# Kernel tuning notes

Measured on AMD Instinct MI355X. Metric: run time of the kernel, lower is better.

The kernel has to match this reference:

```python
import jax, jax.numpy as jnp
import numpy as np

N_NODES = 10000

def setup_inputs() -> dict:
    key = jax.random.key(0)
    k1, k2, k3, k4, k5 = jax.random.split(key, 5)
    n_edges = 640000
    d_in = 128
    d_out = 128
    x = jax.random.normal(k1, (N_NODES, d_in), dtype=jnp.float32)
    src = jax.random.randint(k2, (n_edges,), 0, N_NODES, dtype=jnp.int32)
    dst = jax.random.randint(k3, (n_edges,), 0, N_NODES, dtype=jnp.int32)
    W = jax.random.normal(k4, (d_in, d_out), dtype=jnp.float32) * (1.0 / np.sqrt(d_in))
    b = jax.random.normal(k5, (d_out,), dtype=jnp.float32) * 0.01
    return {"x": x, "src": src, "dst": dst, "W": W, "b": b}

def reference(x, src, dst, W, b):
    # copy_src + sum reduce: for each edge, send x[src]; each node sums incoming msgs
    msgs = x[src]  # [E, d_in] gather
    h = jax.ops.segment_sum(msgs, dst, num_segments=N_NODES)  # [N, d_in] scatter-add
    # dropout p=0.0 -> identity; linear + relu
    out = jax.nn.relu(h @ W + b)  # [N, d_out]
    return out
```

## Files before the change

### kernel.cpp

```cpp
#include <hip/hip_runtime.h>

#define N_NODES 10000
#define D 128
#define N_EDGES 640000
#define SHARDS 8
#define CSTRIDE 10016
#define BCAP 32
#define GEMM_BLOCKS 313
#define FILL_BLOCKS 2500

__device__ __forceinline__ unsigned short f2bf(float f) {
  unsigned int u = __float_as_uint(f);
  unsigned int r = (u + 0x7fffu + ((u >> 16) & 1u)) >> 16;
  return (unsigned short)r;
}
__device__ __forceinline__ float bf2f(unsigned short s) {
  return __uint_as_float((unsigned int)s << 16);
}

__global__ __launch_bounds__(256) void gcn_gemm_histfill_kernel(
    const float* __restrict__ x, const float* __restrict__ W,
    unsigned short* __restrict__ xw,
    const int* __restrict__ src, const int* __restrict__ dst,
    int* __restrict__ counts, unsigned short* __restrict__ srcs_pad) {
  __shared__ unsigned short Wl[D * D];

  if (blockIdx.x >= GEMM_BLOCKS) {
    int e = (blockIdx.x - GEMM_BLOCKS) * 256 + threadIdx.x;
    if (e < N_EDGES) {
      int d = dst[e];
      int s = src[e];
      int sh = blockIdx.x & (SHARDS - 1);
      int r = atomicAdd(&counts[sh * CSTRIDE + d], 1);
      if (r < BCAP)
        srcs_pad[((size_t)d * SHARDS + sh) * BCAP + r] = (unsigned short)s;
    }
    return;
  }

  for (int i = threadIdx.x; i < D * D; i += 256) Wl[i] = f2bf(W[i]);
  __syncthreads();

  const int c0 = (threadIdx.x & 31) * 4;
  const int r0 = blockIdx.x * 32 + (threadIdx.x >> 5) * 4;
  if (r0 >= N_NODES) return;

  float4 acc0 = {0, 0, 0, 0}, acc1 = acc0, acc2 = acc0, acc3 = acc0;
  const float* x0 = x + (size_t)r0 * D;

#define GEMM_STEP(J, HC)                                              \
  {                                                                   \
    ushort4 wu = *(const ushort4*)&Wl[(k4 + J) * D + c0];             \
    float wx = bf2f(wu.x), wy = bf2f(wu.y);                           \
    float wz = bf2f(wu.z), ww = bf2f(wu.w);                           \
    acc0.x = fmaf(hv0.HC, wx, acc0.x);                                \
    acc0.y = fmaf(hv0.HC, wy, acc0.y);                                \
    acc0.z = fmaf(hv0.HC, wz, acc0.z);                                \
    acc0.w = fmaf(hv0.HC, ww, acc0.w);                                \
    acc1.x = fmaf(hv1.HC, wx, acc1.x);                                \
    acc1.y = fmaf(hv1.HC, wy, acc1.y);                                \
    acc1.z = fmaf(hv1.HC, wz, acc1.z);                                \
    acc1.w = fmaf(hv1.HC, ww, acc1.w);                                \
    acc2.x = fmaf(hv2.HC, wx, acc2.x);                                \
    acc2.y = fmaf(hv2.HC, wy, acc2.y);                                \
    acc2.z = fmaf(hv2.HC, wz, acc2.z);                                \
    acc2.w = fmaf(hv2.HC, ww, acc2.w);                                \
    acc3.x = fmaf(hv3.HC, wx, acc3.x);                                \
    acc3.y = fmaf(hv3.HC, wy, acc3.y);                                \
    acc3.z = fmaf(hv3.HC, wz, acc3.z);                                \
    acc3.w = fmaf(hv3.HC, ww, acc3.w);                                \
  }

  for (int k4 = 0; k4 < D; k4 += 4) {
    float4 hv0 = *(const float4*)(x0 + 0 * D + k4);
    float4 hv1 = *(const float4*)(x0 + 1 * D + k4);
    float4 hv2 = *(const float4*)(x0 + 2 * D + k4);
    float4 hv3 = *(const float4*)(x0 + 3 * D + k4);
    GEMM_STEP(0, x)
    GEMM_STEP(1, y)
    GEMM_STEP(2, z)
    GEMM_STEP(3, w)
  }
#undef GEMM_STEP

  ushort4 sv;
#define STORE_ROW(R, ACC)                                              \
  sv.x = f2bf(ACC.x); sv.y = f2bf(ACC.y);                              \
  sv.z = f2bf(ACC.z); sv.w = f2bf(ACC.w);                              \
  *(ushort4*)(xw + (size_t)(r0 + R) * D + c0) = sv;
  STORE_ROW(0, acc0)
  STORE_ROW(1, acc1)
  STORE_ROW(2, acc2)
  STORE_ROW(3, acc3)
#undef STORE_ROW
}

__global__ __launch_bounds__(256) void gcn_gather_kernel(
    const unsigned short* __restrict__ xw, const int* __restrict__ counts,
    const unsigned short* __restrict__ srcs_pad,
    const float* __restrict__ b, float* __restrict__ out) {
  const int node = blockIdx.x * 4 + (threadIdx.x >> 6);
  const int lane = threadIdx.x & 63;

  int c = 0;
  if (lane < SHARDS) c = counts[lane * CSTRIDE + node];

  const unsigned short* npad = srcs_pad + (size_t)node * (SHARDS * BCAP);
  const unsigned int* xw32 = (const unsigned int*)xw;
  float alo = 0.f, ahi = 0.f;

#pragma unroll
  for (int s = 0; s < SHARDS; ++s) {
    int len = __shfl(c, s, 64);
    if (len > BCAP) len = BCAP;
    int id = npad[s * BCAP + (lane & 31)];
    for (int j = 0; j < len; ++j) {
      int sid = __shfl(id, j, 64);
      unsigned int u = xw32[sid * 64 + lane];
      alo += __uint_as_float(u << 16);
      ahi += __uint_as_float(u & 0xffff0000u);
    }
  }

  const float2 bv = *(const float2*)(b + lane * 2);
  float2 o;
  o.x = fmaxf(alo + bv.x, 0.f);
  o.y = fmaxf(ahi + bv.y, 0.f);
  *(float2*)(out + (size_t)node * D + lane * 2) = o;
}

extern "C" void kernel_launch(void* const* d_in, const int* in_sizes, int n_in,
                              void* d_out, int out_size, void* d_ws, size_t ws_size,
                              hipStream_t stream) {
  const float* x   = (const float*)d_in[0];
  const int*   src = (const int*)d_in[1];
  const int*   dst = (const int*)d_in[2];
  const float* W   = (const float*)d_in[3];
  const float* b   = (const float*)d_in[4];
  float* out = (float*)d_out;

  unsigned short* xw       = (unsigned short*)d_ws;
  int*            counts   = (int*)(xw + (size_t)N_NODES * D);
  unsigned short* srcs_pad = (unsigned short*)(counts + SHARDS * CSTRIDE);

  hipMemsetAsync(counts, 0, SHARDS * CSTRIDE * sizeof(int), stream);
  gcn_gemm_histfill_kernel<<<GEMM_BLOCKS + FILL_BLOCKS, 256, 0, stream>>>(
      x, W, xw, src, dst, counts, srcs_pad);
  gcn_gather_kernel<<<N_NODES / 4, 256, 0, stream>>>(xw, counts, srcs_pad, b, out);
}
```

Measured before the change: 139.8 us.

## Fuse memset, GEMM/histogram fill, and gather into one cooperative persistent kernel

Replaces the memset plus two kernel launches with a single cooperative kernel of 1024 persistent blocks. Grid-wide syncs separate three phases: zeroing the counts, GEMM alongside the edge bucketing, and the per-node gather. The aim is to remove launch gaps and the separate memset. In exchange it adds two grid barriers, and the gather loop now runs over fewer blocks. If the cooperative launch fails, it falls back to the original three-step path.

```diff
diff --git a/kernel.cpp b/kernel.cpp
--- a/kernel.cpp
+++ b/kernel.cpp
@@ -1,4 +1,7 @@
 #include <hip/hip_runtime.h>
+#include <hip/hip_cooperative_groups.h>
+
+namespace cg = cooperative_groups;
 
 #define N_NODES 10000
 #define D 128
@@ -7,6 +10,7 @@
 #define CSTRIDE 10016
 #define BCAP 32
 #define GEMM_BLOCKS 313
+#define NBLK 1024
 #define FILL_BLOCKS 2500
 
 __device__ __forceinline__ unsigned short f2bf(float f) {
@@ -18,31 +22,11 @@
   return __uint_as_float((unsigned int)s << 16);
 }
 
-__global__ __launch_bounds__(256) void gcn_gemm_histfill_kernel(
-    const float* __restrict__ x, const float* __restrict__ W,
-    unsigned short* __restrict__ xw,
-    const int* __restrict__ src, const int* __restrict__ dst,
-    int* __restrict__ counts, unsigned short* __restrict__ srcs_pad) {
-  __shared__ unsigned short Wl[D * D];
-
-  if (blockIdx.x >= GEMM_BLOCKS) {
-    int e = (blockIdx.x - GEMM_BLOCKS) * 256 + threadIdx.x;
-    if (e < N_EDGES) {
-      int d = dst[e];
-      int s = src[e];
-      int sh = blockIdx.x & (SHARDS - 1);
-      int r = atomicAdd(&counts[sh * CSTRIDE + d], 1);
-      if (r < BCAP)
-        srcs_pad[((size_t)d * SHARDS + sh) * BCAP + r] = (unsigned short)s;
-    }
-    return;
-  }
-
-  for (int i = threadIdx.x; i < D * D; i += 256) Wl[i] = f2bf(W[i]);
-  __syncthreads();
-
-  const int c0 = (threadIdx.x & 31) * 4;
-  const int r0 = blockIdx.x * 32 + (threadIdx.x >> 5) * 4;
+__device__ __forceinline__ void gemm_block(
+    const float* __restrict__ x, const unsigned short* __restrict__ Wl,
+    unsigned short* __restrict__ xw, int bid, int tid) {
+  const int c0 = (tid & 31) * 4;
+  const int r0 = bid * 32 + (tid >> 5) * 4;
   if (r0 >= N_NODES) return;
 
   float4 acc0 = {0, 0, 0, 0}, acc1 = acc0, acc2 = acc0, acc3 = acc0;
@@ -95,20 +79,14 @@
 #undef STORE_ROW
 }
 
-__global__ __launch_bounds__(256) void gcn_gather_kernel(
-    const unsigned short* __restrict__ xw, const int* __restrict__ counts,
-    const unsigned short* __restrict__ srcs_pad,
-    const float* __restrict__ b, float* __restrict__ out) {
-  const int node = blockIdx.x * 4 + (threadIdx.x >> 6);
-  const int lane = threadIdx.x & 63;
-
+__device__ __forceinline__ void gather_node(
+    const unsigned int* __restrict__ xw32, const int* __restrict__ counts,
+    const unsigned short* __restrict__ srcs_pad, const float* __restrict__ b,
+    float* __restrict__ out, int node, int lane) {
   int c = 0;
   if (lane < SHARDS) c = counts[lane * CSTRIDE + node];
-
   const unsigned short* npad = srcs_pad + (size_t)node * (SHARDS * BCAP);
-  const unsigned int* xw32 = (const unsigned int*)xw;
   float alo = 0.f, ahi = 0.f;
-
 #pragma unroll
   for (int s = 0; s < SHARDS; ++s) {
     int len = __shfl(c, s, 64);
@@ -121,12 +99,86 @@
       ahi += __uint_as_float(u & 0xffff0000u);
     }
   }
-
   const float2 bv = *(const float2*)(b + lane * 2);
   float2 o;
   o.x = fmaxf(alo + bv.x, 0.f);
   o.y = fmaxf(ahi + bv.y, 0.f);
   *(float2*)(out + (size_t)node * D + lane * 2) = o;
+}
+
+__global__ __launch_bounds__(256, 4) void gcn_mega_kernel(
+    const float* __restrict__ x, const float* __restrict__ W,
+    const int* __restrict__ src, const int* __restrict__ dst,
+    const float* __restrict__ b, float* __restrict__ out,
+    unsigned short* __restrict__ xw, int* __restrict__ counts,
+    unsigned short* __restrict__ srcs_pad) {
+  cg::grid_group grid = cg::this_grid();
+  __shared__ unsigned short Wl[D * D];
+
+  {
+    int i = blockIdx.x * 256 + threadIdx.x;
+    if (i < SHARDS * CSTRIDE) counts[i] = 0;
+    if (blockIdx.x < GEMM_BLOCKS)
+      for (int k = threadIdx.x; k < D * D; k += 256) Wl[k] = f2bf(W[k]);
+  }
+  grid.sync();
+
+  if (blockIdx.x < GEMM_BLOCKS) {
+    gemm_block(x, Wl, xw, blockIdx.x, threadIdx.x);
+  } else {
+    const int tbase = (blockIdx.x - GEMM_BLOCKS) * 256 + threadIdx.x;
+    const int tstride = (NBLK - GEMM_BLOCKS) * 256;
+    const int sh = blockIdx.x & (SHARDS - 1);
+    for (int e = tbase; e < N_EDGES; e += tstride) {
+      int d = dst[e];
+      int s = src[e];
+      int r = atomicAdd(&counts[sh * CSTRIDE + d], 1);
+      if (r < BCAP)
+        srcs_pad[((size_t)d * SHARDS + sh) * BCAP + r] = (unsigned short)s;
+    }
+  }
+  grid.sync();
+
+  {
+    const unsigned int* xw32 = (const unsigned int*)xw;
+    const int lane = threadIdx.x & 63;
+    const int sub = threadIdx.x >> 6;
+    for (int g = blockIdx.x; g < N_NODES / 4; g += NBLK) {
+      gather_node(xw32, counts, srcs_pad, b, out, g * 4 + sub, lane);
+    }
+  }
+}
+
+__global__ __launch_bounds__(256) void gcn_gemm_histfill_kernel(
+    const float* __restrict__ x, const float* __restrict__ W,
+    unsigned short* __restrict__ xw,
+    const int* __restrict__ src, const int* __restrict__ dst,
+    int* __restrict__ counts, unsigned short* __restrict__ srcs_pad) {
+  __shared__ unsigned short Wl[D * D];
+  if (blockIdx.x >= GEMM_BLOCKS) {
+    int e = (blockIdx.x - GEMM_BLOCKS) * 256 + threadIdx.x;
+    if (e < N_EDGES) {
+      int d = dst[e];
+      int s = src[e];
+      int sh = blockIdx.x & (SHARDS - 1);
+      int r = atomicAdd(&counts[sh * CSTRIDE + d], 1);
+      if (r < BCAP)
+        srcs_pad[((size_t)d * SHARDS + sh) * BCAP + r] = (unsigned short)s;
+    }
+    return;
+  }
+  for (int i = threadIdx.x; i < D * D; i += 256) Wl[i] = f2bf(W[i]);
+  __syncthreads();
+  gemm_block(x, Wl, xw, blockIdx.x, threadIdx.x);
+}
+
+__global__ __launch_bounds__(256) void gcn_gather_kernel(
+    const unsigned short* __restrict__ xw, const int* __restrict__ counts,
+    const unsigned short* __restrict__ srcs_pad,
+    const float* __restrict__ b, float* __restrict__ out) {
+  const int node = blockIdx.x * 4 + (threadIdx.x >> 6);
+  const int lane = threadIdx.x & 63;
+  gather_node((const unsigned int*)xw, counts, srcs_pad, b, out, node, lane);
 }
 
 extern "C" void kernel_launch(void* const* d_in, const int* in_sizes, int n_in,
@@ -143,8 +195,15 @@
   int*            counts   = (int*)(xw + (size_t)N_NODES * D);
   unsigned short* srcs_pad = (unsigned short*)(counts + SHARDS * CSTRIDE);
 
-  hipMemsetAsync(counts, 0, SHARDS * CSTRIDE * sizeof(int), stream);
-  gcn_gemm_histfill_kernel<<<GEMM_BLOCKS + FILL_BLOCKS, 256, 0, stream>>>(
-      x, W, xw, src, dst, counts, srcs_pad);
-  gcn_gather_kernel<<<N_NODES / 4, 256, 0, stream>>>(xw, counts, srcs_pad, b, out);
-}
+  void* args[] = {(void*)&x, (void*)&W, (void*)&src, (void*)&dst, (void*)&b,
+                  (void*)&out, (void*)&xw, (void*)&counts, (void*)&srcs_pad};
+  hipError_t err = hipLaunchCooperativeKernel(
+      (const void*)gcn_mega_kernel, dim3(NBLK), dim3(256), args, 0, stream);
+
+  if (err != hipSuccess) {
+    hipMemsetAsync(counts, 0, SHARDS * CSTRIDE * sizeof(int), stream);
+    gcn_gemm_histfill_kernel<<<GEMM_BLOCKS + FILL_BLOCKS, 256, 0, stream>>>(
+        x, W, xw, src, dst, counts, srcs_pad);
+    gcn_gather_kernel<<<N_NODES / 4, 256, 0, stream>>>(xw, counts, srcs_pad, b, out);
+  }
+}
```

After: 375.5 us. +168.6%, slower.

## Split histogram fill into separate kernel, widen to 16 shards, unroll gather

Applied to the files above, without the earlier changes.

Moves the edge-bucketing work out of the fused GEMM kernel into its own kernel, where each thread handles four edges through vectorized int4 loads. The shard count rises from 8 to 16 to spread atomic contention across more counters. The gather loop is unrolled by two so two row loads can be in flight at once. In exchange, the GEMM and fill no longer overlap within one launch, an extra kernel launch is added, and the gather now reads 16 shard counts per node.

```diff
diff --git a/kernel.cpp b/kernel.cpp
--- a/kernel.cpp
+++ b/kernel.cpp
@@ -3,11 +3,10 @@
 #define N_NODES 10000
 #define D 128
 #define N_EDGES 640000
-#define SHARDS 8
+#define SHARDS 16
 #define CSTRIDE 10016
 #define BCAP 32
 #define GEMM_BLOCKS 313
-#define FILL_BLOCKS 2500
 
 __device__ __forceinline__ unsigned short f2bf(float f) {
   unsigned int u = __float_as_uint(f);
@@ -18,26 +17,10 @@
   return __uint_as_float((unsigned int)s << 16);
 }
 
-__global__ __launch_bounds__(256) void gcn_gemm_histfill_kernel(
+__global__ __launch_bounds__(256) void gcn_gemm_kernel(
     const float* __restrict__ x, const float* __restrict__ W,
-    unsigned short* __restrict__ xw,
-    const int* __restrict__ src, const int* __restrict__ dst,
-    int* __restrict__ counts, unsigned short* __restrict__ srcs_pad) {
+    unsigned short* __restrict__ xw) {
   __shared__ unsigned short Wl[D * D];
-
-  if (blockIdx.x >= GEMM_BLOCKS) {
-    int e = (blockIdx.x - GEMM_BLOCKS) * 256 + threadIdx.x;
-    if (e < N_EDGES) {
-      int d = dst[e];
-      int s = src[e];
-      int sh = blockIdx.x & (SHARDS - 1);
-      int r = atomicAdd(&counts[sh * CSTRIDE + d], 1);
-      if (r < BCAP)
-        srcs_pad[((size_t)d * SHARDS + sh) * BCAP + r] = (unsigned short)s;
-    }
-    return;
-  }
-
   for (int i = threadIdx.x; i < D * D; i += 256) Wl[i] = f2bf(W[i]);
   __syncthreads();
 
@@ -95,6 +78,25 @@
 #undef STORE_ROW
 }
 
+__global__ __launch_bounds__(256) void gcn_histfill_kernel(
+    const int* __restrict__ src, const int* __restrict__ dst,
+    int* __restrict__ counts, unsigned short* __restrict__ srcs_pad) {
+  const int e4 = (blockIdx.x * 256 + threadIdx.x) * 4;
+  const int sh = blockIdx.x & (SHARDS - 1);
+  const int4 d4 = *(const int4*)(dst + e4);
+  const int4 s4 = *(const int4*)(src + e4);
+  int* csh = counts + sh * CSTRIDE;
+
+  int r0 = atomicAdd(&csh[d4.x], 1);
+  int r1 = atomicAdd(&csh[d4.y], 1);
+  int r2 = atomicAdd(&csh[d4.z], 1);
+  int r3 = atomicAdd(&csh[d4.w], 1);
+  if (r0 < BCAP) srcs_pad[((size_t)d4.x * SHARDS + sh) * BCAP + r0] = (unsigned short)s4.x;
+  if (r1 < BCAP) srcs_pad[((size_t)d4.y * SHARDS + sh) * BCAP + r1] = (unsigned short)s4.y;
+  if (r2 < BCAP) srcs_pad[((size_t)d4.z * SHARDS + sh) * BCAP + r2] = (unsigned short)s4.z;
+  if (r3 < BCAP) srcs_pad[((size_t)d4.w * SHARDS + sh) * BCAP + r3] = (unsigned short)s4.w;
+}
+
 __global__ __launch_bounds__(256) void gcn_gather_kernel(
     const unsigned short* __restrict__ xw, const int* __restrict__ counts,
     const unsigned short* __restrict__ srcs_pad,
@@ -114,7 +116,18 @@
     int len = __shfl(c, s, 64);
     if (len > BCAP) len = BCAP;
     int id = npad[s * BCAP + (lane & 31)];
-    for (int j = 0; j < len; ++j) {
+    int j = 0;
+    for (; j + 2 <= len; j += 2) {
+      int sid0 = __shfl(id, j, 64);
+      int sid1 = __shfl(id, j + 1, 64);
+      unsigned int u0 = xw32[sid0 * 64 + lane];
+      unsigned int u1 = xw32[sid1 * 64 + lane];
+      alo += __uint_as_float(u0 << 16);
+      ahi += __uint_as_float(u0 & 0xffff0000u);
+      alo += __uint_as_float(u1 << 16);
+      ahi += __uint_as_float(u1 & 0xffff0000u);
+    }
+    if (j < len) {
       int sid = __shfl(id, j, 64);
       unsigned int u = xw32[sid * 64 + lane];
       alo += __uint_as_float(u << 16);
@@ -144,7 +157,7 @@
   unsigned short* srcs_pad = (unsigned short*)(counts + SHARDS * CSTRIDE);
 
   hipMemsetAsync(counts, 0, SHARDS * CSTRIDE * sizeof(int), stream);
-  gcn_gemm_histfill_kernel<<<GEMM_BLOCKS + FILL_BLOCKS, 256, 0, stream>>>(
-      x, W, xw, src, dst, counts, srcs_pad);
+  gcn_gemm_kernel<<<GEMM_BLOCKS, 256, 0, stream>>>(x, W, xw);
+  gcn_histfill_kernel<<<N_EDGES / (256 * 4), 256, 0, stream>>>(src, dst, counts, srcs_pad);
   gcn_gather_kernel<<<N_NODES / 4, 256, 0, stream>>>(xw, counts, srcs_pad, b, out);
 }
```

Result: slower. 144.0 us (+3.0%).
